# Kernel optimization log

Measured on AMD Instinct MI355X. Metric: run time of the kernel, lower is better.

## Reference

```python
import jax, jax.numpy as jnp
import numpy as np

B = 262144      # batch (many robot-timestep samples)
IN_LEN = 32     # input_len
S = 64          # internal_state_len
M = 32          # message_len
P = 4           # num_ports
H = 100         # hidden_layer_size
L = 50          # lstm_hidden_size
O = 16          # output_len


def _linear_init(key, out_f, in_f):
    # torch.nn.Linear default init: U(-1/sqrt(in_f), 1/sqrt(in_f)) for W and b
    kw, kb = jax.random.split(key)
    bound = 1.0 / np.sqrt(in_f)
    W = jax.random.uniform(kw, (out_f, in_f), jnp.float32, -bound, bound)
    b = jax.random.uniform(kb, (out_f,), jnp.float32, -bound, bound)
    return W, b


def setup_inputs() -> dict:
    key = jax.random.key(0)
    ks = jax.random.split(key, 20)
    obs = jax.random.normal(ks[0], (B, IN_LEN), jnp.float32)
    messages_in = jax.random.normal(ks[1], (P, B, M), jnp.float32)
    h_lstm = jax.random.normal(ks[2], (B, L), jnp.float32)
    c_lstm = jax.random.normal(ks[3], (B, L), jnp.float32)

    W_in, b_in = _linear_init(ks[4], S, IN_LEN)
    # per-port message MLPs, stacked on a leading port axis
    msg1 = [_linear_init(jax.random.fold_in(ks[5], p), H, S) for p in range(P)]
    msg2 = [_linear_init(jax.random.fold_in(ks[6], p), M, H) for p in range(P)]
    msg_W1 = jnp.stack([w for w, _ in msg1])  # [P, H, S]
    msg_b1 = jnp.stack([b for _, b in msg1])  # [P, H]
    msg_W2 = jnp.stack([w for w, _ in msg2])  # [P, M, H]
    msg_b2 = jnp.stack([b for _, b in msg2])  # [P, M]

    # LSTMCell(S + M*P -> L); torch gate order i, f, g, o; init U(-1/sqrt(L), 1/sqrt(L))
    bl = 1.0 / np.sqrt(L)
    W_ih = jax.random.uniform(ks[7], (4 * L, S + M * P), jnp.float32, -bl, bl)
    W_hh = jax.random.uniform(ks[8], (4 * L, L), jnp.float32, -bl, bl)
    b_ih = jax.random.uniform(ks[9], (4 * L,), jnp.float32, -bl, bl)
    b_hh = jax.random.uniform(ks[10], (4 * L,), jnp.float32, -bl, bl)

    W_u1, b_u1 = _linear_init(ks[11], H, L)
    W_u2, b_u2 = _linear_init(ks[12], H, H)
    W_u3, b_u3 = _linear_init(ks[13], S, H)
    W_mu, b_mu = _linear_init(ks[14], O, S)
    W_var, b_var = _linear_init(ks[15], O, S)
    max_logvar = jnp.ones((1, O), jnp.float32) / 2.0
    min_logvar = -jnp.ones((1, O), jnp.float32) * 10.0

    return dict(obs=obs, messages_in=messages_in, h_lstm=h_lstm, c_lstm=c_lstm,
                W_in=W_in, b_in=b_in, msg_W1=msg_W1, msg_b1=msg_b1,
                msg_W2=msg_W2, msg_b2=msg_b2, W_ih=W_ih, W_hh=W_hh,
                b_ih=b_ih, b_hh=b_hh, W_u1=W_u1, b_u1=b_u1, W_u2=W_u2,
                b_u2=b_u2, W_u3=W_u3, b_u3=b_u3, W_mu=W_mu, b_mu=b_mu,
                W_var=W_var, b_var=b_var, max_logvar=max_logvar,
                min_logvar=min_logvar)


def reference(obs, messages_in, h_lstm, c_lstm, W_in, b_in, msg_W1, msg_b1,
              msg_W2, msg_b2, W_ih, W_hh, b_ih, b_hh, W_u1, b_u1, W_u2, b_u2,
              W_u3, b_u3, W_mu, b_mu, W_var, b_var, max_logvar, min_logvar):
    # run_input_function
    x = jax.nn.relu(obs @ W_in.T + b_in)                       # [B, S]

    # compute_messages_out_function: batched over ports (all ports occupied)
    m1 = jax.nn.relu(jnp.einsum('bs,phs->pbh', x, msg_W1) + msg_b1[:, None, :])
    msgs_out = jnp.einsum('pbh,pmh->pbm', m1, msg_W2) + msg_b2[:, None, :]  # [P, B, M]

    # compute_aggregation_function: concat incoming messages along feature dim
    agg = jnp.transpose(messages_in, (1, 0, 2)).reshape(obs.shape[0], -1)  # [B, P*M]
    h_mbar = jnp.concatenate([x, agg], axis=-1)                # [B, S + P*M]

    # status_update_function: one LSTMCell step (torch gate order i, f, g, o)
    gates = h_mbar @ W_ih.T + b_ih + h_lstm @ W_hh.T + b_hh    # [B, 4L]
    i, f, g, o = jnp.split(gates, 4, axis=-1)
    c_new = jax.nn.sigmoid(f) * c_lstm + jax.nn.sigmoid(i) * jnp.tanh(g)
    h_new = jax.nn.sigmoid(o) * jnp.tanh(c_new)                # [B, L]
    h2 = jax.nn.relu(h_new @ W_u1.T + b_u1)
    h2 = jax.nn.relu(h2 @ W_u2.T + b_u2)
    h2 = h2 @ W_u3.T + b_u3                                    # new internal state [B, S]

    # compute_output_function with soft logvar clamping
    mu = h2 @ W_mu.T + b_mu                                    # [B, O]
    logvar = h2 @ W_var.T + b_var
    logvar = max_logvar - jax.nn.softplus(max_logvar - logvar)
    logvar = min_logvar + jax.nn.softplus(logvar - min_logvar)
    var = jnp.exp(logvar)

    msgs_flat = jnp.transpose(msgs_out, (1, 0, 2)).reshape(obs.shape[0], -1)  # [B, P*M]
    # concat all outputs: mu(16) var(16) msgs(128) h2(64) h_new(50) c_new(50) = 324
    return jnp.concatenate([mu, var, msgs_flat, h2, h_new, c_new], axis=-1)
```

## Files before the change

### kernel.cpp

```cpp
#include <hip/hip_runtime.h>

typedef __bf16 bf16_t;
typedef __bf16 bf16x8 __attribute__((ext_vector_type(8)));
typedef float f32x4 __attribute__((ext_vector_type(4)));

#define B_TOTAL 262144
#define OUTC 324

#define OFF_WIN   0
#define OFF_WG    2048
#define OFF_WM1   67584
#define OFF_WM2   96256
#define OFF_WU1   112640
#define OFF_WU2   119808
#define OFF_WU3   134144
#define OFF_WMV   142336
#define BF16_TOTAL 144384

__global__ void prep_kernel(const float* W_in, const float* msg_W1, const float* msg_W2,
                            const float* W_ih, const float* W_hh, const float* b_ih, const float* b_hh,
                            const float* W_u1, const float* W_u2, const float* W_u3,
                            const float* W_mu, const float* W_var,
                            bf16_t* wb, float* bg) {
  int tid = blockIdx.x * blockDim.x + threadIdx.x;
  int nth = gridDim.x * blockDim.x;
  for (int i = tid; i < 2048; i += nth) wb[OFF_WIN + i] = (bf16_t)W_in[i];
  for (int i = tid; i < 65536; i += nth) {
    int n = i >> 8, k = i & 255;
    int g = n >> 6, j = n & 63;
    float v = 0.f;
    if (j < 50) {
      int r = g * 50 + j;
      if (k < 192) v = W_ih[r * 192 + k];
      else if (k < 242) v = W_hh[r * 50 + (k - 192)];
    }
    wb[OFF_WG + i] = (bf16_t)v;
  }
  for (int i = tid; i < 256; i += nth) {
    int g = i >> 6, j = i & 63;
    bg[i] = (j < 50) ? (b_ih[g * 50 + j] + b_hh[g * 50 + j]) : 0.f;
  }
  for (int i = tid; i < 4 * 112 * 64; i += nth) {
    int p = i / (112 * 64); int rem = i % (112 * 64); int n = rem >> 6, k = rem & 63;
    wb[OFF_WM1 + i] = (bf16_t)((n < 100) ? msg_W1[(p * 100 + n) * 64 + k] : 0.f);
  }
  for (int i = tid; i < 4 * 32 * 128; i += nth) {
    int p = i / (32 * 128); int rem = i % (32 * 128); int n = rem >> 7, k = rem & 127;
    wb[OFF_WM2 + i] = (bf16_t)((k < 100) ? msg_W2[(p * 32 + n) * 100 + k] : 0.f);
  }
  for (int i = tid; i < 112 * 64; i += nth) {
    int n = i >> 6, k = i & 63;
    wb[OFF_WU1 + i] = (bf16_t)((n < 100 && k < 50) ? W_u1[n * 50 + k] : 0.f);
  }
  for (int i = tid; i < 112 * 128; i += nth) {
    int n = i >> 7, k = i & 127;
    wb[OFF_WU2 + i] = (bf16_t)((n < 100 && k < 100) ? W_u2[n * 100 + k] : 0.f);
  }
  for (int i = tid; i < 64 * 128; i += nth) {
    int n = i >> 7, k = i & 127;
    wb[OFF_WU3 + i] = (bf16_t)((k < 100) ? W_u3[n * 100 + k] : 0.f);
  }
  for (int i = tid; i < 32 * 64; i += nth) {
    int n = i >> 6, k = i & 63;
    wb[OFF_WMV + i] = (bf16_t)((n < 16) ? W_mu[n * 64 + k] : W_var[(n - 16) * 64 + k]);
  }
}

template <int KS>
__device__ __forceinline__ f32x4 mm_tile(const bf16_t* A, int lda,
                                         const bf16_t* Bw, int ldb,
                                         f32x4 acc, int lr, int kq) {
  const bf16_t* ap = A + lr * lda + kq * 8;
  const bf16_t* bp = Bw + lr * ldb + kq * 8;
#pragma unroll
  for (int k = 0; k < KS; k++) {
    bf16x8 a = *(const bf16x8*)(ap + k * 32);
    bf16x8 b = *(const bf16x8*)(bp + k * 32);
    acc = __builtin_amdgcn_mfma_f32_16x16x32_bf16(a, b, acc, 0, 0, 0);
  }
  return acc;
}

__device__ __forceinline__ float softplus_f(float x) {
  return (x > 20.f) ? x : log1pf(expf(x));
}

__global__ __launch_bounds__(256, 2) void fused_kernel(
    const float* __restrict__ obs, const float* __restrict__ msg_in,
    const float* __restrict__ h_lstm, const float* __restrict__ c_lstm,
    const float* __restrict__ b_in, const float* __restrict__ msg_b1,
    const float* __restrict__ msg_b2, const float* __restrict__ b_u1,
    const float* __restrict__ b_u2, const float* __restrict__ b_u3,
    const float* __restrict__ b_mu, const float* __restrict__ b_var,
    const float* __restrict__ maxlv, const float* __restrict__ minlv,
    const bf16_t* __restrict__ wb, const float* __restrict__ bg,
    float* __restrict__ out) {
  __shared__ __align__(16) bf16_t hm[64 * 264];
  __shared__ __align__(16) bf16_t t1[64 * 136];
  __shared__ __align__(16) bf16_t hn[64 * 72];

  const int tid = threadIdx.x;
  const int row0 = blockIdx.x * 64;
  const int lane = tid & 63;
  const int wave = tid >> 6;
  const int lr = lane & 15;
  const int kq = lane >> 4;
  bf16_t* obs_l = t1;

  {
    int base = tid * 8;
    int row = base >> 5, col = base & 31;
    const float4* s = (const float4*)(obs + (size_t)row0 * 32 + base);
    float4 v0 = s[0], v1 = s[1];
    bf16_t* d = obs_l + row * 40 + col;
    d[0] = (bf16_t)v0.x; d[1] = (bf16_t)v0.y; d[2] = (bf16_t)v0.z; d[3] = (bf16_t)v0.w;
    d[4] = (bf16_t)v1.x; d[5] = (bf16_t)v1.y; d[6] = (bf16_t)v1.z; d[7] = (bf16_t)v1.w;
  }
#pragma unroll
  for (int p = 0; p < 4; p++) {
    int base = tid * 8;
    int row = base >> 5, m = base & 31;
    const float4* s = (const float4*)(msg_in + (size_t)p * B_TOTAL * 32 + (size_t)row0 * 32 + base);
    float4 v0 = s[0], v1 = s[1];
    bf16_t* d = hm + row * 264 + 64 + p * 32 + m;
    d[0] = (bf16_t)v0.x; d[1] = (bf16_t)v0.y; d[2] = (bf16_t)v0.z; d[3] = (bf16_t)v0.w;
    d[4] = (bf16_t)v1.x; d[5] = (bf16_t)v1.y; d[6] = (bf16_t)v1.z; d[7] = (bf16_t)v1.w;
  }
  {
    int base = tid * 16;
    int row = base >> 6, c0 = base & 63;
    const float* s = h_lstm + (size_t)(row0 + row) * 50;
    bf16_t* d = hm + row * 264 + 192;
#pragma unroll
    for (int i = 0; i < 16; i++) {
      int c = c0 + i;
      d[c] = (bf16_t)((c < 50) ? s[c] : 0.f);
    }
  }
  __syncthreads();

  {
    int nb = wave * 16;
    float bv = b_in[nb + lr];
    const bf16_t* Bw = wb + OFF_WIN + nb * 32;
#pragma unroll
    for (int m = 0; m < 4; m++) {
      f32x4 acc = {bv, bv, bv, bv};
      acc = mm_tile<1>(obs_l + m * 16 * 40, 40, Bw, 32, acc, lr, kq);
#pragma unroll
      for (int rr = 0; rr < 4; rr++) {
        float v = acc[rr]; v = v > 0.f ? v : 0.f;
        hm[(m * 16 + kq * 4 + rr) * 264 + nb + lr] = (bf16_t)v;
      }
    }
  }
  __syncthreads();

  {
    int idx = tid * 4;
    int row = idx >> 4;
    int cc = 112 + (idx & 15);
#pragma unroll
    for (int q = 0; q < 4; q++) t1[row * 136 + cc + q] = (bf16_t)0.f;
  }

  for (int p = 0; p < 4; p++) {
    for (int nt = wave; nt < 7; nt += 4) {
      int nb = nt * 16;
      float bv = (nb + lr < 100) ? msg_b1[p * 100 + nb + lr] : 0.f;
      const bf16_t* Bw = wb + OFF_WM1 + p * 112 * 64 + nb * 64;
#pragma unroll
      for (int m = 0; m < 4; m++) {
        f32x4 acc = {bv, bv, bv, bv};
        acc = mm_tile<2>(hm + m * 16 * 264, 264, Bw, 64, acc, lr, kq);
#pragma unroll
        for (int rr = 0; rr < 4; rr++) {
          float v = acc[rr]; v = v > 0.f ? v : 0.f;
          t1[(m * 16 + kq * 4 + rr) * 136 + nb + lr] = (bf16_t)v;
        }
      }
    }
    __syncthreads();
#pragma unroll
    for (int nt = 0; nt < 2; nt++) {
      int nb = nt * 16;
      int m = wave;
      float bv = msg_b2[p * 32 + nb + lr];
      const bf16_t* Bw = wb + OFF_WM2 + p * 32 * 128 + nb * 128;
      f32x4 acc = {bv, bv, bv, bv};
      acc = mm_tile<4>(t1 + m * 16 * 136, 136, Bw, 128, acc, lr, kq);
#pragma unroll
      for (int rr = 0; rr < 4; rr++) {
        int row = row0 + m * 16 + kq * 4 + rr;
        out[(size_t)row * OUTC + 32 + p * 32 + nb + lr] = acc[rr];
      }
    }
    __syncthreads();
  }

  {
    const bf16_t* Bg = wb + OFF_WG;
    const int nbase = wave * 16 + lr;
    bf16x8 Bf0[8], Bf1[8], Bf2[8], Bf3[8];
#pragma unroll
    for (int k = 0; k < 8; k++) {
      Bf0[k] = *(const bf16x8*)(Bg + (0 * 64 + nbase) * 256 + kq * 8 + k * 32);
      Bf1[k] = *(const bf16x8*)(Bg + (1 * 64 + nbase) * 256 + kq * 8 + k * 32);
      Bf2[k] = *(const bf16x8*)(Bg + (2 * 64 + nbase) * 256 + kq * 8 + k * 32);
      Bf3[k] = *(const bf16x8*)(Bg + (3 * 64 + nbase) * 256 + kq * 8 + k * 32);
    }
    float bv0 = bg[nbase], bv1 = bg[64 + nbase], bv2 = bg[128 + nbase], bv3 = bg[192 + nbase];
    const int j = nbase;
#pragma unroll
    for (int m = 0; m < 4; m++) {
      bf16x8 Af[8];
#pragma unroll
      for (int k = 0; k < 8; k++)
        Af[k] = *(const bf16x8*)(hm + (m * 16 + lr) * 264 + kq * 8 + k * 32);
      f32x4 ai = {bv0, bv0, bv0, bv0}, af = {bv1, bv1, bv1, bv1};
      f32x4 ag = {bv2, bv2, bv2, bv2}, ao = {bv3, bv3, bv3, bv3};
#pragma unroll
      for (int k = 0; k < 8; k++) {
        ai = __builtin_amdgcn_mfma_f32_16x16x32_bf16(Af[k], Bf0[k], ai, 0, 0, 0);
        af = __builtin_amdgcn_mfma_f32_16x16x32_bf16(Af[k], Bf1[k], af, 0, 0, 0);
        ag = __builtin_amdgcn_mfma_f32_16x16x32_bf16(Af[k], Bf2[k], ag, 0, 0, 0);
        ao = __builtin_amdgcn_mfma_f32_16x16x32_bf16(Af[k], Bf3[k], ao, 0, 0, 0);
      }
#pragma unroll
      for (int rr = 0; rr < 4; rr++) {
        int lrow = m * 16 + kq * 4 + rr;
        int row = row0 + lrow;
        float iv = ai[rr], fv = af[rr], gv = ag[rr], ov = ao[rr];
        float c_old = 0.f;
        if (j < 50) c_old = c_lstm[(size_t)row * 50 + j];
        float si = 1.f / (1.f + expf(-iv));
        float sf = 1.f / (1.f + expf(-fv));
        float so = 1.f / (1.f + expf(-ov));
        float cn = sf * c_old + si * tanhf(gv);
        float hv = so * tanhf(cn);
        if (j < 50) {
          out[(size_t)row * OUTC + 274 + j] = cn;
          out[(size_t)row * OUTC + 224 + j] = hv;
        }
        hn[lrow * 72 + j] = (bf16_t)((j < 50) ? hv : 0.f);
      }
    }
  }
  __syncthreads();

  {
    int idx = tid * 4;
    int row = idx >> 4;
    int cc = 176 + (idx & 15);
#pragma unroll
    for (int q = 0; q < 4; q++) hm[row * 264 + cc + q] = (bf16_t)0.f;
  }

  for (int nt = wave; nt < 7; nt += 4) {
    int nb = nt * 16;
    float bv = (nb + lr < 100) ? b_u1[nb + lr] : 0.f;
    const bf16_t* Bw = wb + OFF_WU1 + nb * 64;
#pragma unroll
    for (int m = 0; m < 4; m++) {
      f32x4 acc = {bv, bv, bv, bv};
      acc = mm_tile<2>(hn + m * 16 * 72, 72, Bw, 64, acc, lr, kq);
#pragma unroll
      for (int rr = 0; rr < 4; rr++) {
        float v = acc[rr]; v = v > 0.f ? v : 0.f;
        t1[(m * 16 + kq * 4 + rr) * 136 + nb + lr] = (bf16_t)v;
      }
    }
  }
  __syncthreads();

  for (int nt = wave; nt < 7; nt += 4) {
    int nb = nt * 16;
    float bv = (nb + lr < 100) ? b_u2[nb + lr] : 0.f;
    const bf16_t* Bw = wb + OFF_WU2 + nb * 128;
#pragma unroll
    for (int m = 0; m < 4; m++) {
      f32x4 acc = {bv, bv, bv, bv};
      acc = mm_tile<4>(t1 + m * 16 * 136, 136, Bw, 128, acc, lr, kq);
#pragma unroll
      for (int rr = 0; rr < 4; rr++) {
        float v = acc[rr]; v = v > 0.f ? v : 0.f;
        hm[(m * 16 + kq * 4 + rr) * 264 + 64 + nb + lr] = (bf16_t)v;
      }
    }
  }
  __syncthreads();

  {
    int nb = wave * 16;
    float bv = b_u3[nb + lr];
    const bf16_t* Bw = wb + OFF_WU3 + nb * 128;
#pragma unroll
    for (int m = 0; m < 4; m++) {
      f32x4 acc = {bv, bv, bv, bv};
      acc = mm_tile<4>(hm + m * 16 * 264 + 64, 264, Bw, 128, acc, lr, kq);
#pragma unroll
      for (int rr = 0; rr < 4; rr++) {
        int lrow = m * 16 + kq * 4 + rr;
        int row = row0 + lrow;
        float v = acc[rr];
        out[(size_t)row * OUTC + 160 + nb + lr] = v;
        t1[lrow * 136 + nb + lr] = (bf16_t)v;
      }
    }
  }
  __syncthreads();

  {
    int m = wave;
    const bf16_t* Ab = t1 + m * 16 * 136;
    {
      float bv = b_mu[lr];
      f32x4 acc = {bv, bv, bv, bv};
      acc = mm_tile<2>(Ab, 136, wb + OFF_WMV, 64, acc, lr, kq);
#pragma unroll
      for (int rr = 0; rr < 4; rr++) {
        int row = row0 + m * 16 + kq * 4 + rr;
        out[(size_t)row * OUTC + lr] = acc[rr];
      }
    }
    {
      float bv = b_var[lr];
      f32x4 acc = {bv, bv, bv, bv};
      acc = mm_tile<2>(Ab, 136, wb + OFF_WMV + 16 * 64, 64, acc, lr, kq);
      float mx = maxlv[lr], mn = minlv[lr];
#pragma unroll
      for (int rr = 0; rr < 4; rr++) {
        int row = row0 + m * 16 + kq * 4 + rr;
        float lv = acc[rr];
        lv = mx - softplus_f(mx - lv);
        lv = mn + softplus_f(lv - mn);
        out[(size_t)row * OUTC + 16 + lr] = expf(lv);
      }
    }
  }
}

extern "C" void kernel_launch(void* const* d_in, const int* in_sizes, int n_in,
                              void* d_out, int out_size, void* d_ws, size_t ws_size,
                              hipStream_t stream) {
  const float* obs   = (const float*)d_in[0];
  const float* msgs  = (const float*)d_in[1];
  const float* h_l   = (const float*)d_in[2];
  const float* c_l   = (const float*)d_in[3];
  const float* W_in  = (const float*)d_in[4];
  const float* b_in  = (const float*)d_in[5];
  const float* mW1   = (const float*)d_in[6];
  const float* mb1   = (const float*)d_in[7];
  const float* mW2   = (const float*)d_in[8];
  const float* mb2   = (const float*)d_in[9];
  const float* W_ih  = (const float*)d_in[10];
  const float* W_hh  = (const float*)d_in[11];
  const float* b_ih  = (const float*)d_in[12];
  const float* b_hh  = (const float*)d_in[13];
  const float* W_u1  = (const float*)d_in[14];
  const float* b_u1  = (const float*)d_in[15];
  const float* W_u2  = (const float*)d_in[16];
  const float* b_u2  = (const float*)d_in[17];
  const float* W_u3  = (const float*)d_in[18];
  const float* b_u3  = (const float*)d_in[19];
  const float* W_mu  = (const float*)d_in[20];
  const float* b_mu  = (const float*)d_in[21];
  const float* W_var = (const float*)d_in[22];
  const float* b_var = (const float*)d_in[23];
  const float* maxlv = (const float*)d_in[24];
  const float* minlv = (const float*)d_in[25];

  bf16_t* wb = (bf16_t*)d_ws;
  float* bg = (float*)((char*)d_ws + (size_t)BF16_TOTAL * 2);

  prep_kernel<<<64, 256, 0, stream>>>(W_in, mW1, mW2, W_ih, W_hh, b_ih, b_hh,
                                      W_u1, W_u2, W_u3, W_mu, W_var, wb, bg);
  fused_kernel<<<B_TOTAL / 64, 256, 0, stream>>>(
      obs, msgs, h_l, c_l, b_in, mb1, mb2, b_u1, b_u2, b_u3,
      b_mu, b_var, maxlv, minlv, wb, bg, (float*)d_out);
}
```

Baseline: 402.8 us.

## Halve rows per block, raise occupancy, vectorize staging, use fast transcendentals

Each block now handles 32 rows instead of 64, with smaller LDS tiles and launch bounds raised to 4 blocks per SU. The LSTM gate weights are loaded per gate inside the loop rather than all held in registers. Input staging uses packed 16-byte bf16 stores, and the A fragments for the message layer are hoisted out of the port loop. Sigmoid, tanh, softplus and exp switch to fast intrinsics built on rcp. Together these aim to lift occupancy and latency hiding, at the cost of more weight reloads per row and slightly lower accuracy in the activations.

```diff
diff --git a/kernel.cpp b/kernel.cpp
--- a/kernel.cpp
+++ b/kernel.cpp
@@ -6,6 +6,7 @@
 
 #define B_TOTAL 262144
 #define OUTC 324
+#define ROWS 32
 
 #define OFF_WIN   0
 #define OFF_WG    2048
@@ -66,26 +67,14 @@
   }
 }
 
-template <int KS>
-__device__ __forceinline__ f32x4 mm_tile(const bf16_t* A, int lda,
-                                         const bf16_t* Bw, int ldb,
-                                         f32x4 acc, int lr, int kq) {
-  const bf16_t* ap = A + lr * lda + kq * 8;
-  const bf16_t* bp = Bw + lr * ldb + kq * 8;
-#pragma unroll
-  for (int k = 0; k < KS; k++) {
-    bf16x8 a = *(const bf16x8*)(ap + k * 32);
-    bf16x8 b = *(const bf16x8*)(bp + k * 32);
-    acc = __builtin_amdgcn_mfma_f32_16x16x32_bf16(a, b, acc, 0, 0, 0);
-  }
-  return acc;
-}
-
-__device__ __forceinline__ float softplus_f(float x) {
-  return (x > 20.f) ? x : log1pf(expf(x));
-}
-
-__global__ __launch_bounds__(256, 2) void fused_kernel(
+#define MFMA(a, b, c) __builtin_amdgcn_mfma_f32_16x16x32_bf16((a), (b), (c), 0, 0, 0)
+
+__device__ __forceinline__ float frcp(float x) { return __builtin_amdgcn_rcpf(x); }
+__device__ __forceinline__ float fsigmoid(float x) { return frcp(1.f + __expf(-x)); }
+__device__ __forceinline__ float ftanh_f(float x) { return 1.f - 2.f * frcp(1.f + __expf(2.f * x)); }
+__device__ __forceinline__ float fsoftplus(float x) { return (x > 15.f) ? x : __logf(1.f + __expf(x)); }
+
+__global__ __launch_bounds__(256, 4) void fused_kernel(
     const float* __restrict__ obs, const float* __restrict__ msg_in,
     const float* __restrict__ h_lstm, const float* __restrict__ c_lstm,
     const float* __restrict__ b_in, const float* __restrict__ msg_b1,
@@ -95,152 +84,172 @@
     const float* __restrict__ maxlv, const float* __restrict__ minlv,
     const bf16_t* __restrict__ wb, const float* __restrict__ bg,
     float* __restrict__ out) {
-  __shared__ __align__(16) bf16_t hm[64 * 264];
-  __shared__ __align__(16) bf16_t t1[64 * 136];
-  __shared__ __align__(16) bf16_t hn[64 * 72];
+  __shared__ __align__(16) bf16_t hm[ROWS * 264];
+  __shared__ __align__(16) bf16_t t1[ROWS * 136];
+  __shared__ __align__(16) bf16_t hn[ROWS * 72];
 
   const int tid = threadIdx.x;
-  const int row0 = blockIdx.x * 64;
+  const int row0 = blockIdx.x * ROWS;
   const int lane = tid & 63;
-  const int wave = tid >> 6;
+  const int w = tid >> 6;
   const int lr = lane & 15;
   const int kq = lane >> 4;
   bf16_t* obs_l = t1;
 
-  {
+  if (tid < 128) {
     int base = tid * 8;
     int row = base >> 5, col = base & 31;
     const float4* s = (const float4*)(obs + (size_t)row0 * 32 + base);
     float4 v0 = s[0], v1 = s[1];
-    bf16_t* d = obs_l + row * 40 + col;
-    d[0] = (bf16_t)v0.x; d[1] = (bf16_t)v0.y; d[2] = (bf16_t)v0.z; d[3] = (bf16_t)v0.w;
-    d[4] = (bf16_t)v1.x; d[5] = (bf16_t)v1.y; d[6] = (bf16_t)v1.z; d[7] = (bf16_t)v1.w;
-  }
-#pragma unroll
+    bf16x8 pk;
+    pk[0] = (bf16_t)v0.x; pk[1] = (bf16_t)v0.y; pk[2] = (bf16_t)v0.z; pk[3] = (bf16_t)v0.w;
+    pk[4] = (bf16_t)v1.x; pk[5] = (bf16_t)v1.y; pk[6] = (bf16_t)v1.z; pk[7] = (bf16_t)v1.w;
+    *(bf16x8*)(obs_l + row * 40 + col) = pk;
+  }
+  {
+    int i = tid * 16;
+    int p = i >> 10, rem = i & 1023;
+    int row = rem >> 5, col = rem & 31;
+    const float4* s = (const float4*)(msg_in + (size_t)p * B_TOTAL * 32 + (size_t)(row0 + row) * 32 + col);
+    float4 v0 = s[0], v1 = s[1], v2 = s[2], v3 = s[3];
+    bf16x8 a, b;
+    a[0] = (bf16_t)v0.x; a[1] = (bf16_t)v0.y; a[2] = (bf16_t)v0.z; a[3] = (bf16_t)v0.w;
+    a[4] = (bf16_t)v1.x; a[5] = (bf16_t)v1.y; a[6] = (bf16_t)v1.z; a[7] = (bf16_t)v1.w;
+    b[0] = (bf16_t)v2.x; b[1] = (bf16_t)v2.y; b[2] = (bf16_t)v2.z; b[3] = (bf16_t)v2.w;
+    b[4] = (bf16_t)v3.x; b[5] = (bf16_t)v3.y; b[6] = (bf16_t)v3.z; b[7] = (bf16_t)v3.w;
+    bf16_t* d = hm + row * 264 + 64 + p * 32 + col;
+    *(bf16x8*)d = a;
+    *(bf16x8*)(d + 8) = b;
+  }
+  {
+    int i = tid * 8;
+    int row = i >> 6, c0 = i & 63;
+    const float* s = h_lstm + (size_t)(row0 + row) * 50 + c0;
+    bf16x8 pk;
+#pragma unroll
+    for (int q = 0; q < 8; q++) {
+      float v = 0.f;
+      if (c0 + q < 50) v = s[q];
+      pk[q] = (bf16_t)v;
+    }
+    *(bf16x8*)(hm + row * 264 + 192 + c0) = pk;
+  }
+  __syncthreads();
+
+  {
+    int nb = w * 16;
+    float bv = b_in[nb + lr];
+    bf16x8 B0 = *(const bf16x8*)(wb + OFF_WIN + (nb + lr) * 32 + kq * 8);
+#pragma unroll
+    for (int m = 0; m < 2; m++) {
+      bf16x8 A0 = *(const bf16x8*)(obs_l + (m * 16 + lr) * 40 + kq * 8);
+      f32x4 acc = {bv, bv, bv, bv};
+      acc = MFMA(A0, B0, acc);
+#pragma unroll
+      for (int rr = 0; rr < 4; rr++)
+        hm[(m * 16 + kq * 4 + rr) * 264 + nb + lr] = (bf16_t)fmaxf(acc[rr], 0.f);
+    }
+  }
+  __syncthreads();
+
+  if (tid < 64) {
+    int row = tid >> 1, c = 112 + (tid & 1) * 8;
+    bf16x8 z = {};
+    *(bf16x8*)(t1 + row * 136 + c) = z;
+  }
+
+  bf16x8 ax[2][2];
+#pragma unroll
+  for (int m = 0; m < 2; m++)
+#pragma unroll
+    for (int k = 0; k < 2; k++)
+      ax[m][k] = *(const bf16x8*)(hm + (m * 16 + lr) * 264 + kq * 8 + k * 32);
+
   for (int p = 0; p < 4; p++) {
-    int base = tid * 8;
-    int row = base >> 5, m = base & 31;
-    const float4* s = (const float4*)(msg_in + (size_t)p * B_TOTAL * 32 + (size_t)row0 * 32 + base);
-    float4 v0 = s[0], v1 = s[1];
-    bf16_t* d = hm + row * 264 + 64 + p * 32 + m;
-    d[0] = (bf16_t)v0.x; d[1] = (bf16_t)v0.y; d[2] = (bf16_t)v0.z; d[3] = (bf16_t)v0.w;
-    d[4] = (bf16_t)v1.x; d[5] = (bf16_t)v1.y; d[6] = (bf16_t)v1.z; d[7] = (bf16_t)v1.w;
-  }
-  {
-    int base = tid * 16;
-    int row = base >> 6, c0 = base & 63;
-    const float* s = h_lstm + (size_t)(row0 + row) * 50;
-    bf16_t* d = hm + row * 264 + 192;
-#pragma unroll
-    for (int i = 0; i < 16; i++) {
-      int c = c0 + i;
-      d[c] = (bf16_t)((c < 50) ? s[c] : 0.f);
-    }
-  }
-  __syncthreads();
-
-  {
-    int nb = wave * 16;
-    float bv = b_in[nb + lr];
-    const bf16_t* Bw = wb + OFF_WIN + nb * 32;
-#pragma unroll
-    for (int m = 0; m < 4; m++) {
-      f32x4 acc = {bv, bv, bv, bv};
-      acc = mm_tile<1>(obs_l + m * 16 * 40, 40, Bw, 32, acc, lr, kq);
-#pragma unroll
-      for (int rr = 0; rr < 4; rr++) {
-        float v = acc[rr]; v = v > 0.f ? v : 0.f;
-        hm[(m * 16 + kq * 4 + rr) * 264 + nb + lr] = (bf16_t)v;
-      }
-    }
-  }
-  __syncthreads();
-
-  {
-    int idx = tid * 4;
-    int row = idx >> 4;
-    int cc = 112 + (idx & 15);
-#pragma unroll
-    for (int q = 0; q < 4; q++) t1[row * 136 + cc + q] = (bf16_t)0.f;
-  }
-
-  for (int p = 0; p < 4; p++) {
-    for (int nt = wave; nt < 7; nt += 4) {
+    for (int nt = w; nt < 7; nt += 4) {
       int nb = nt * 16;
       float bv = (nb + lr < 100) ? msg_b1[p * 100 + nb + lr] : 0.f;
-      const bf16_t* Bw = wb + OFF_WM1 + p * 112 * 64 + nb * 64;
-#pragma unroll
-      for (int m = 0; m < 4; m++) {
+      const bf16_t* Bp = wb + OFF_WM1 + p * 112 * 64 + (nb + lr) * 64 + kq * 8;
+      bf16x8 b0 = *(const bf16x8*)Bp;
+      bf16x8 b1 = *(const bf16x8*)(Bp + 32);
+#pragma unroll
+      for (int m = 0; m < 2; m++) {
         f32x4 acc = {bv, bv, bv, bv};
-        acc = mm_tile<2>(hm + m * 16 * 264, 264, Bw, 64, acc, lr, kq);
-#pragma unroll
-        for (int rr = 0; rr < 4; rr++) {
-          float v = acc[rr]; v = v > 0.f ? v : 0.f;
-          t1[(m * 16 + kq * 4 + rr) * 136 + nb + lr] = (bf16_t)v;
-        }
+        acc = MFMA(ax[m][0], b0, acc);
+        acc = MFMA(ax[m][1], b1, acc);
+#pragma unroll
+        for (int rr = 0; rr < 4; rr++)
+          t1[(m * 16 + kq * 4 + rr) * 136 + nb + lr] = (bf16_t)fmaxf(acc[rr], 0.f);
       }
     }
     __syncthreads();
-#pragma unroll
-    for (int nt = 0; nt < 2; nt++) {
+    {
+      int nt = w & 1, m = w >> 1;
       int nb = nt * 16;
-      int m = wave;
       float bv = msg_b2[p * 32 + nb + lr];
-      const bf16_t* Bw = wb + OFF_WM2 + p * 32 * 128 + nb * 128;
-      f32x4 acc = {bv, bv, bv, bv};
-      acc = mm_tile<4>(t1 + m * 16 * 136, 136, Bw, 128, acc, lr, kq);
-#pragma unroll
-      for (int rr = 0; rr < 4; rr++) {
-        int row = row0 + m * 16 + kq * 4 + rr;
-        out[(size_t)row * OUTC + 32 + p * 32 + nb + lr] = acc[rr];
+      const bf16_t* Bp = wb + OFF_WM2 + p * 32 * 128 + (nb + lr) * 128 + kq * 8;
+      f32x4 acc = {bv, bv, bv, bv};
+#pragma unroll
+      for (int k = 0; k < 4; k++) {
+        bf16x8 a = *(const bf16x8*)(t1 + (m * 16 + lr) * 136 + kq * 8 + k * 32);
+        bf16x8 b = *(const bf16x8*)(Bp + k * 32);
+        acc = MFMA(a, b, acc);
+      }
+#pragma unroll
+      for (int rr = 0; rr < 4; rr++) {
+        size_t row = row0 + m * 16 + kq * 4 + rr;
+        out[row * OUTC + 32 + p * 32 + nb + lr] = acc[rr];
       }
     }
     __syncthreads();
   }
 
   {
-    const bf16_t* Bg = wb + OFF_WG;
-    const int nbase = wave * 16 + lr;
-    bf16x8 Bf0[8], Bf1[8], Bf2[8], Bf3[8];
-#pragma unroll
-    for (int k = 0; k < 8; k++) {
-      Bf0[k] = *(const bf16x8*)(Bg + (0 * 64 + nbase) * 256 + kq * 8 + k * 32);
-      Bf1[k] = *(const bf16x8*)(Bg + (1 * 64 + nbase) * 256 + kq * 8 + k * 32);
-      Bf2[k] = *(const bf16x8*)(Bg + (2 * 64 + nbase) * 256 + kq * 8 + k * 32);
-      Bf3[k] = *(const bf16x8*)(Bg + (3 * 64 + nbase) * 256 + kq * 8 + k * 32);
-    }
-    float bv0 = bg[nbase], bv1 = bg[64 + nbase], bv2 = bg[128 + nbase], bv3 = bg[192 + nbase];
-    const int j = nbase;
-#pragma unroll
-    for (int m = 0; m < 4; m++) {
-      bf16x8 Af[8];
+    const int j = w * 16 + lr;
+    float c_pre[2][4];
+#pragma unroll
+    for (int m = 0; m < 2; m++)
+#pragma unroll
+      for (int rr = 0; rr < 4; rr++) {
+        size_t row = row0 + m * 16 + kq * 4 + rr;
+        float cv = 0.f;
+        if (j < 50) cv = c_lstm[row * 50 + j];
+        c_pre[m][rr] = cv;
+      }
+    float bb0 = bg[j], bb1 = bg[64 + j], bb2 = bg[128 + j], bb3 = bg[192 + j];
+#pragma unroll
+    for (int m = 0; m < 2; m++) {
+      bf16x8 a[8];
 #pragma unroll
       for (int k = 0; k < 8; k++)
-        Af[k] = *(const bf16x8*)(hm + (m * 16 + lr) * 264 + kq * 8 + k * 32);
-      f32x4 ai = {bv0, bv0, bv0, bv0}, af = {bv1, bv1, bv1, bv1};
-      f32x4 ag = {bv2, bv2, bv2, bv2}, ao = {bv3, bv3, bv3, bv3};
-#pragma unroll
-      for (int k = 0; k < 8; k++) {
-        ai = __builtin_amdgcn_mfma_f32_16x16x32_bf16(Af[k], Bf0[k], ai, 0, 0, 0);
-        af = __builtin_amdgcn_mfma_f32_16x16x32_bf16(Af[k], Bf1[k], af, 0, 0, 0);
-        ag = __builtin_amdgcn_mfma_f32_16x16x32_bf16(Af[k], Bf2[k], ag, 0, 0, 0);
-        ao = __builtin_amdgcn_mfma_f32_16x16x32_bf16(Af[k], Bf3[k], ao, 0, 0, 0);
+        a[k] = *(const bf16x8*)(hm + (m * 16 + lr) * 264 + kq * 8 + k * 32);
+      f32x4 ai = {bb0, bb0, bb0, bb0}, af = {bb1, bb1, bb1, bb1};
+      f32x4 ag = {bb2, bb2, bb2, bb2}, ao = {bb3, bb3, bb3, bb3};
+#pragma unroll
+      for (int g = 0; g < 4; g++) {
+        bf16x8 bfr[8];
+#pragma unroll
+        for (int k = 0; k < 8; k++)
+          bfr[k] = *(const bf16x8*)(wb + OFF_WG + (size_t)(g * 64 + j) * 256 + kq * 8 + k * 32);
+        f32x4* accp = (g == 0) ? &ai : (g == 1) ? &af : (g == 2) ? &ag : &ao;
+        f32x4 acc = *accp;
+#pragma unroll
+        for (int k = 0; k < 8; k++) acc = MFMA(a[k], bfr[k], acc);
+        *accp = acc;
       }
 #pragma unroll
       for (int rr = 0; rr < 4; rr++) {
         int lrow = m * 16 + kq * 4 + rr;
-        int row = row0 + lrow;
-        float iv = ai[rr], fv = af[rr], gv = ag[rr], ov = ao[rr];
-        float c_old = 0.f;
-        if (j < 50) c_old = c_lstm[(size_t)row * 50 + j];
-        float si = 1.f / (1.f + expf(-iv));
-        float sf = 1.f / (1.f + expf(-fv));
-        float so = 1.f / (1.f + expf(-ov));
-        float cn = sf * c_old + si * tanhf(gv);
-        float hv = so * tanhf(cn);
+        size_t row = row0 + lrow;
+        float si = fsigmoid(ai[rr]);
+        float sf = fsigmoid(af[rr]);
+        float gv = ftanh_f(ag[rr]);
+        float so = fsigmoid(ao[rr]);
+        float cn = sf * c_pre[m][rr] + si * gv;
+        float hv = so * ftanh_f(cn);
         if (j < 50) {
-          out[(size_t)row * OUTC + 274 + j] = cn;
-          out[(size_t)row * OUTC + 224 + j] = hv;
+          out[row * OUTC + 274 + j] = cn;
+          out[row * OUTC + 224 + j] = hv;
         }
         hn[lrow * 72 + j] = (bf16_t)((j < 50) ? hv : 0.f);
       }
@@ -248,93 +257,116 @@
   }
   __syncthreads();
 
-  {
-    int idx = tid * 4;
-    int row = idx >> 4;
-    int cc = 176 + (idx & 15);
-#pragma unroll
-    for (int q = 0; q < 4; q++) hm[row * 264 + cc + q] = (bf16_t)0.f;
-  }
-
-  for (int nt = wave; nt < 7; nt += 4) {
-    int nb = nt * 16;
-    float bv = (nb + lr < 100) ? b_u1[nb + lr] : 0.f;
-    const bf16_t* Bw = wb + OFF_WU1 + nb * 64;
-#pragma unroll
-    for (int m = 0; m < 4; m++) {
-      f32x4 acc = {bv, bv, bv, bv};
-      acc = mm_tile<2>(hn + m * 16 * 72, 72, Bw, 64, acc, lr, kq);
-#pragma unroll
-      for (int rr = 0; rr < 4; rr++) {
-        float v = acc[rr]; v = v > 0.f ? v : 0.f;
-        t1[(m * 16 + kq * 4 + rr) * 136 + nb + lr] = (bf16_t)v;
-      }
-    }
-  }
-  __syncthreads();
-
-  for (int nt = wave; nt < 7; nt += 4) {
+  if (tid < 64) {
+    int row = tid >> 1, c = 176 + (tid & 1) * 8;
+    bf16x8 z = {};
+    *(bf16x8*)(hm + row * 264 + c) = z;
+  }
+
+  {
+    bf16x8 ah[2][2];
+#pragma unroll
+    for (int m = 0; m < 2; m++)
+#pragma unroll
+      for (int k = 0; k < 2; k++)
+        ah[m][k] = *(const bf16x8*)(hn + (m * 16 + lr) * 72 + kq * 8 + k * 32);
+    for (int nt = w; nt < 7; nt += 4) {
+      int nb = nt * 16;
+      float bv = (nb + lr < 100) ? b_u1[nb + lr] : 0.f;
+      const bf16_t* Bp = wb + OFF_WU1 + (nb + lr) * 64 + kq * 8;
+      bf16x8 b0 = *(const bf16x8*)Bp;
+      bf16x8 b1 = *(const bf16x8*)(Bp + 32);
+#pragma unroll
+      for (int m = 0; m < 2; m++) {
+        f32x4 acc = {bv, bv, bv, bv};
+        acc = MFMA(ah[m][0], b0, acc);
+        acc = MFMA(ah[m][1], b1, acc);
+#pragma unroll
+        for (int rr = 0; rr < 4; rr++)
+          t1[(m * 16 + kq * 4 + rr) * 136 + nb + lr] = (bf16_t)fmaxf(acc[rr], 0.f);
+      }
+    }
+  }
+  __syncthreads();
+
+  for (int nt = w; nt < 7; nt += 4) {
     int nb = nt * 16;
     float bv = (nb + lr < 100) ? b_u2[nb + lr] : 0.f;
-    const bf16_t* Bw = wb + OFF_WU2 + nb * 128;
-#pragma unroll
-    for (int m = 0; m < 4; m++) {
-      f32x4 acc = {bv, bv, bv, bv};
-      acc = mm_tile<4>(t1 + m * 16 * 136, 136, Bw, 128, acc, lr, kq);
-#pragma unroll
-      for (int rr = 0; rr < 4; rr++) {
-        float v = acc[rr]; v = v > 0.f ? v : 0.f;
-        hm[(m * 16 + kq * 4 + rr) * 264 + 64 + nb + lr] = (bf16_t)v;
-      }
-    }
-  }
-  __syncthreads();
-
-  {
-    int nb = wave * 16;
+    const bf16_t* Bp = wb + OFF_WU2 + (nb + lr) * 128 + kq * 8;
+    bf16x8 bb[4];
+#pragma unroll
+    for (int k = 0; k < 4; k++) bb[k] = *(const bf16x8*)(Bp + k * 32);
+#pragma unroll
+    for (int m = 0; m < 2; m++) {
+      f32x4 acc = {bv, bv, bv, bv};
+#pragma unroll
+      for (int k = 0; k < 4; k++) {
+        bf16x8 a = *(const bf16x8*)(t1 + (m * 16 + lr) * 136 + kq * 8 + k * 32);
+        acc = MFMA(a, bb[k], acc);
+      }
+#pragma unroll
+      for (int rr = 0; rr < 4; rr++)
+        hm[(m * 16 + kq * 4 + rr) * 264 + 64 + nb + lr] = (bf16_t)fmaxf(acc[rr], 0.f);
+    }
+  }
+  __syncthreads();
+
+  {
+    int nb = w * 16;
     float bv = b_u3[nb + lr];
-    const bf16_t* Bw = wb + OFF_WU3 + nb * 128;
-#pragma unroll
-    for (int m = 0; m < 4; m++) {
-      f32x4 acc = {bv, bv, bv, bv};
-      acc = mm_tile<4>(hm + m * 16 * 264 + 64, 264, Bw, 128, acc, lr, kq);
+    const bf16_t* Bp = wb + OFF_WU3 + (nb + lr) * 128 + kq * 8;
+    bf16x8 bb[4];
+#pragma unroll
+    for (int k = 0; k < 4; k++) bb[k] = *(const bf16x8*)(Bp + k * 32);
+#pragma unroll
+    for (int m = 0; m < 2; m++) {
+      f32x4 acc = {bv, bv, bv, bv};
+#pragma unroll
+      for (int k = 0; k < 4; k++) {
+        bf16x8 a = *(const bf16x8*)(hm + (m * 16 + lr) * 264 + 64 + kq * 8 + k * 32);
+        acc = MFMA(a, bb[k], acc);
+      }
 #pragma unroll
       for (int rr = 0; rr < 4; rr++) {
         int lrow = m * 16 + kq * 4 + rr;
-        int row = row0 + lrow;
-        float v = acc[rr];
-        out[(size_t)row * OUTC + 160 + nb + lr] = v;
-        t1[lrow * 136 + nb + lr] = (bf16_t)v;
-      }
-    }
-  }
-  __syncthreads();
-
-  {
-    int m = wave;
-    const bf16_t* Ab = t1 + m * 16 * 136;
-    {
+        size_t row = row0 + lrow;
+        out[row * OUTC + 160 + nb + lr] = acc[rr];
+        t1[lrow * 136 + nb + lr] = (bf16_t)acc[rr];
+      }
+    }
+  }
+  __syncthreads();
+
+  {
+    int m = w & 1, head = w >> 1;
+    const bf16_t* Bp = wb + OFF_WMV + head * 16 * 64 + lr * 64 + kq * 8;
+    bf16x8 b0 = *(const bf16x8*)Bp;
+    bf16x8 b1 = *(const bf16x8*)(Bp + 32);
+    bf16x8 a0 = *(const bf16x8*)(t1 + (m * 16 + lr) * 136 + kq * 8);
+    bf16x8 a1 = *(const bf16x8*)(t1 + (m * 16 + lr) * 136 + kq * 8 + 32);
+    if (head == 0) {
       float bv = b_mu[lr];
       f32x4 acc = {bv, bv, bv, bv};
-      acc = mm_tile<2>(Ab, 136, wb + OFF_WMV, 64, acc, lr, kq);
-#pragma unroll
-      for (int rr = 0; rr < 4; rr++) {
-        int row = row0 + m * 16 + kq * 4 + rr;
-        out[(size_t)row * OUTC + lr] = acc[rr];
-      }
-    }
-    {
+      acc = MFMA(a0, b0, acc);
+      acc = MFMA(a1, b1, acc);
+#pragma unroll
+      for (int rr = 0; rr < 4; rr++) {
+        size_t row = row0 + m * 16 + kq * 4 + rr;
+        out[row * OUTC + lr] = acc[rr];
+      }
+    } else {
       float bv = b_var[lr];
       f32x4 acc = {bv, bv, bv, bv};
-      acc = mm_tile<2>(Ab, 136, wb + OFF_WMV + 16 * 64, 64, acc, lr, kq);
+      acc = MFMA(a0, b0, acc);
+      acc = MFMA(a1, b1, acc);
       float mx = maxlv[lr], mn = minlv[lr];
 #pragma unroll
       for (int rr = 0; rr < 4; rr++) {
-        int row = row0 + m * 16 + kq * 4 + rr;
+        size_t row = row0 + m * 16 + kq * 4 + rr;
         float lv = acc[rr];
-        lv = mx - softplus_f(mx - lv);
-        lv = mn + softplus_f(lv - mn);
-        out[(size_t)row * OUTC + 16 + lr] = expf(lv);
+        lv = mx - fsoftplus(mx - lv);
+        lv = mn + fsoftplus(lv - mn);
+        out[row * OUTC + 16 + lr] = __expf(lv);
       }
     }
   }
@@ -375,7 +407,7 @@
 
   prep_kernel<<<64, 256, 0, stream>>>(W_in, mW1, mW2, W_ih, W_hh, b_ih, b_hh,
                                       W_u1, W_u2, W_u3, W_mu, W_var, wb, bg);
-  fused_kernel<<<B_TOTAL / 64, 256, 0, stream>>>(
+  fused_kernel<<<B_TOTAL / ROWS, 256, 0, stream>>>(
       obs, msgs, h_l, c_l, b_in, mb1, mb2, b_u1, b_u2, b_u3,
       b_mu, b_var, maxlv, minlv, wb, bg, (float*)d_out);
 }
```

Result: slower. 508.9 us (+26.4%).
